# Kernel optimization log

Measured on AMD Instinct MI355X. Metric: run time of the kernel, lower is better.

The kernel has to match this reference:

```python
import jax, jax.numpy as jnp
import numpy as np

B, T, N, V, C, E = 64, 100, 25, 128, 128, 64
EPS = 1e-5


def setup_inputs() -> dict:
    key = jax.random.key(0)
    ks = jax.random.split(key, 6)
    x = jax.random.normal(ks[0], (B, T, N, V), jnp.float32)
    edge_index = jax.random.randint(ks[1], (2, E), 0, N, dtype=jnp.int64)
    W1 = jax.random.normal(ks[2], (V, C), jnp.float32) * (1.0 / np.sqrt(V))
    b1 = jnp.zeros((C,), jnp.float32)
    W2 = jax.random.normal(ks[3], (C, C), jnp.float32) * (1.0 / np.sqrt(C))
    b2 = jnp.zeros((C,), jnp.float32)
    gamma = jnp.ones((T,), jnp.float32)
    beta = jnp.zeros((T,), jnp.float32)
    return {"x": x, "edge_index": edge_index, "W1": W1, "b1": b1,
            "W2": W2, "b2": b2, "gamma": gamma, "beta": beta}


def _gcn_norm(edge_index, n):
    # GCNConv default: add self-loops, symmetric D^{-1/2} A_hat D^{-1/2} norm.
    loop = jnp.arange(n, dtype=edge_index.dtype)
    src = jnp.concatenate([edge_index[0], loop])  # [E + N]
    tgt = jnp.concatenate([edge_index[1], loop])
    deg = jnp.zeros((n,), jnp.float32).at[tgt].add(1.0)
    dis = jax.lax.rsqrt(deg)  # deg >= 1 due to self-loops
    return src, tgt, dis[src] * dis[tgt]


def _gcn_layer(h, W, b, src, tgt, norm):
    # h: [G, N, Cin] -> [G, N, Cout]; linear then gather-scale-scatter aggregate.
    h = jnp.einsum('gnc,cd->gnd', h, W)
    msg = h[:, src, :] * norm[None, :, None]          # [G, E+N, Cout]
    out = jnp.zeros_like(h).at[:, tgt, :].add(msg)    # scatter-add to targets
    return out + b


def reference(x, edge_index, W1, b1, W2, b2, gamma, beta):
    Bv, Tv, Nv, Vv = x.shape
    h = x.reshape(Bv * Tv, Nv, Vv)  # B*T independent graphs, shared edge_index
    src, tgt, norm = _gcn_norm(edge_index, Nv)
    h = _gcn_layer(h, W1, b1, src, tgt, norm)
    h = _gcn_layer(h, W2, b2, src, tgt, norm)
    y = h.reshape(Bv, Tv, Nv, -1)
    # BatchNorm2d(T) in training mode: batch stats over (B, N, C) per T-channel.
    mean = y.mean(axis=(0, 2, 3), keepdims=True)
    var = y.var(axis=(0, 2, 3), keepdims=True)  # biased, matches torch normalization
    y = (y - mean) * jax.lax.rsqrt(var + EPS)
    y = y * gamma[None, :, None, None] + beta[None, :, None, None]
    return jax.nn.relu(y)
```

## Files before the change

### kernel.cpp

```cpp
#include <hip/hip_runtime.h>

#define T_DIM   100
#define N_NODES 25
#define C_DIM   128
#define G_TOTAL 6400
#define GNV     3200
#define TOT_ELEM 20480000
#define CNT_PER_T 204800.0f

#define WS_A2P  0
#define WS_RS1  640
#define WS_BW   768
#define WS_SUM  1024
#define WS_SSQ  1152
#define WS_W12T 2048
#define WS_HB   16384

#define YSTR  36
#define YGSTR (128 * YSTR)

typedef __attribute__((ext_vector_type(8))) short short8;
typedef __attribute__((ext_vector_type(4))) float f32x4;

__device__ __forceinline__ unsigned short f2bf(float f) {
  unsigned int u = __float_as_uint(f);
  u += 0x7FFFu + ((u >> 16) & 1u);
  return (unsigned short)(u >> 16);
}
__device__ __forceinline__ float bf2f(unsigned short h) {
  return __uint_as_float(((unsigned int)h) << 16);
}
__device__ __forceinline__ unsigned int pack2bf(float a, float b) {
  return (unsigned int)f2bf(a) | ((unsigned int)f2bf(b) << 16);
}

__global__ void k_pre(const int* __restrict__ edge, const float* __restrict__ W1,
                      const float* __restrict__ W2, const float* __restrict__ b1,
                      float* __restrict__ wsf) {
  __shared__ float sA[N_NODES * N_NODES];
  __shared__ float sA2[N_NODES * N_NODES];
  __shared__ float sdeg[N_NODES];
  __shared__ float sdis[N_NODES];
  const int tid = threadIdx.x;

  if (blockIdx.x < 64) {
    int j = blockIdx.x * 256 + tid;
    int c = j & 127, v = j >> 7;
    float acc = 0.f;
#pragma unroll 8
    for (int u = 0; u < 128; u++) acc = fmaf(W1[v * 128 + u], W2[u * 128 + c], acc);
    ((unsigned short*)(wsf + WS_W12T))[c * 128 + v] = f2bf(acc);
    if (j < 128) {
      float a2 = 0.f;
      for (int u = 0; u < 128; u++) a2 = fmaf(W2[u * 128 + j], b1[u], a2);
      wsf[WS_BW + j] = a2;
    }
    return;
  }

  if (tid < N_NODES) sdeg[tid] = 0.f;
  for (int j = tid; j < N_NODES * N_NODES; j += 256) sA[j] = 0.f;
  __syncthreads();
  if (tid < 64) atomicAdd(&sdeg[edge[64 + tid]], 1.f);
  __syncthreads();
  if (tid < N_NODES) sdis[tid] = rsqrtf(sdeg[tid] + 1.f);
  __syncthreads();
  if (tid < 64) {
    int s = edge[tid], tg = edge[64 + tid];
    atomicAdd(&sA[tg * N_NODES + s], sdis[s] * sdis[tg]);
  }
  __syncthreads();
  if (tid < N_NODES) atomicAdd(&sA[tid * N_NODES + tid], sdis[tid] * sdis[tid]);
  __syncthreads();
  for (int j = tid; j < N_NODES * N_NODES; j += 256) {
    int n = j / N_NODES, m = j - n * N_NODES;
    float acc = 0.f;
    for (int k = 0; k < N_NODES; k++) acc = fmaf(sA[n * N_NODES + k], sA[k * N_NODES + m], acc);
    sA2[j] = acc;
  }
  __syncthreads();
  for (int j = tid; j < 1024; j += 256) {
    int m = j >> 5, k = j & 31;
    float v = (m < N_NODES && k < N_NODES) ? sA2[m * N_NODES + k] : 0.f;
    ((unsigned short*)(wsf + WS_A2P))[j] = f2bf(v);
  }
  if (tid < N_NODES) {
    float rs = 0.f;
    for (int m = 0; m < N_NODES; m++) rs += sA[tid * N_NODES + m];
    wsf[WS_RS1 + tid] = rs;
  }
  if (tid < T_DIM) { wsf[WS_SUM + tid] = 0.f; wsf[WS_SSQ + tid] = 0.f; }
}

__device__ __forceinline__ void load_a2f(const unsigned short* __restrict__ A2p,
                                         int quad, int l16, short8 a2f[2]) {
#pragma unroll
  for (int mt2 = 0; mt2 < 2; mt2++)
    a2f[mt2] = *(const short8*)&A2p[(mt2 * 16 + l16) * 32 + quad * 8];
}

template <int NT>
__device__ __forceinline__ void stage_x_global(unsigned short* __restrict__ LB,
                                               const float* __restrict__ xb, int tid) {
  for (int j = tid; j < 12 * 128; j += NT) {
    int pr = j >> 7;
    int g = pr / 3, rr = pr - (pr / 3) * 3;
    LB[(g * 28 + 25 + rr) * 128 + (j & 127)] = 0;
  }
  for (int idx = tid; idx < 1600; idx += NT) {
    int row = idx >> 4;
    int c8  = (idx & 15) << 3;
    int g = (row * 41) >> 10;
    int n = row - g * 25;
    const float4* xp = (const float4*)(xb + g * (T_DIM * GNV) + n * 128 + c8);
    float4 f0 = xp[0], f1 = xp[1];
    uint4 w;
    w.x = pack2bf(f0.x, f0.y); w.y = pack2bf(f0.z, f0.w);
    w.z = pack2bf(f1.x, f1.y); w.w = pack2bf(f1.z, f1.w);
    int r = g * 28 + n;
    *(uint4*)&LB[r * 128 + (c8 ^ ((r & 15) << 3))] = w;
  }
}

__device__ __forceinline__ void do_stage2_half(const unsigned short* __restrict__ LB,
    const short8 a2f[2], const float* __restrict__ sBW, const float* __restrict__ sB2,
    const float* __restrict__ rs1, unsigned short* __restrict__ hb, int obase,
    int g, int half, int quad, int l16, float& sum, float& ssq) {
  f32x4 acc2[2][4];
#pragma unroll
  for (int mt2 = 0; mt2 < 2; mt2++)
#pragma unroll
    for (int nt = 0; nt < 4; nt++)
#pragma unroll
      for (int r = 0; r < 4; r++) acc2[mt2][nt][r] = 0.f;

#pragma unroll
  for (int nt = 0; nt < 4; nt++) {
    int c = (half * 4 + nt) * 16 + l16;
    int base = g * YGSTR + c * YSTR + quad * 8;
    uint2 lo = *(const uint2*)&LB[base];
    uint2 hi = *(const uint2*)&LB[base + 4];
    uint4 w; w.x = lo.x; w.y = lo.y; w.z = hi.x; w.w = hi.y;
    short8 bf = __builtin_bit_cast(short8, w);
#pragma unroll
    for (int mt2 = 0; mt2 < 2; mt2++)
      acc2[mt2][nt] = __builtin_amdgcn_mfma_f32_16x16x32_bf16(a2f[mt2], bf, acc2[mt2][nt], 0, 0, 0);
  }
#pragma unroll
  for (int mt2 = 0; mt2 < 2; mt2++) {
#pragma unroll
    for (int nt = 0; nt < 4; nt++) {
      int c = (half * 4 + nt) * 16 + l16;
      float bw = sBW[c], bb = sB2[c];
#pragma unroll
      for (int r = 0; r < 4; r++) {
        int m = mt2 * 16 + quad * 4 + r;
        if (m < N_NODES) {
          float v = acc2[mt2][nt][r] + rs1[m] * bw + bb;
          unsigned short hv = f2bf(v);
          float vq = bf2f(hv);
          hb[obase + m * 128 + c] = hv;
          sum += vq;
          ssq += vq * vq;
        }
      }
    }
  }
}

__global__ __launch_bounds__(512, 8) void k_main_w8(const float* __restrict__ x,
                                                    const float* __restrict__ b2,
                                                    const float* __restrict__ wsc,
                                                    float* __restrict__ stats,
                                                    unsigned short* __restrict__ hb) {
  __shared__ __align__(16) unsigned short LB[4 * YGSTR];
  __shared__ float sBW[128];
  __shared__ float sB2[128];
  __shared__ float rs1[32];
  __shared__ float red[16];
  const int tid = threadIdx.x;
  const int bid = blockIdx.x;
  const int t = bid % T_DIM;
  const int bq = bid / T_DIM;
  const int wv = tid >> 6, lane = tid & 63, quad = lane >> 4, l16 = lane & 15;
  const unsigned short* Wg = (const unsigned short*)(wsc + WS_W12T);
  const unsigned short* A2p = (const unsigned short*)(wsc + WS_A2P);

  if (tid < 128) {
    sBW[tid] = wsc[WS_BW + tid];
    if (tid < N_NODES) rs1[tid] = wsc[WS_RS1 + tid];
  } else if (tid < 256) {
    sB2[tid - 128] = b2[tid - 128];
  }

  stage_x_global<512>(LB, x + (bq * 4 * T_DIM + t) * GNV, tid);

  short8 bfr[4];
  {
    const short8* rp = (const short8*)&Wg[(wv * 16 + l16) * 128];
#pragma unroll
    for (int ks = 0; ks < 4; ks++) bfr[ks] = rp[(ks << 2) | quad];
  }
  __syncthreads();

  f32x4 acc[7];
#pragma unroll
  for (int mt = 0; mt < 7; mt++)
#pragma unroll
    for (int r = 0; r < 4; r++) acc[mt][r] = 0.f;

#pragma unroll
  for (int ks = 0; ks < 4; ks++) {
    const int cc = (ks << 2) | quad;
#pragma unroll
    for (int mt = 0; mt < 7; mt++) {
      int arow = mt * 16 + l16;
      short8 afr = *(const short8*)&LB[arow * 128 + ((cc ^ (arow & 15)) << 3)];
      acc[mt] = __builtin_amdgcn_mfma_f32_16x16x32_bf16(afr, bfr[ks], acc[mt], 0, 0, 0);
    }
  }
  __syncthreads();

#pragma unroll
  for (int mt = 0; mt < 7; mt++) {
    int row0 = mt * 16 + quad * 4;
    int g = row0 / 28;
    int rl = row0 - g * 28;
    int c = wv * 16 + l16;
    uint2 p;
    p.x = pack2bf(acc[mt][0], acc[mt][1]);
    p.y = pack2bf(acc[mt][2], acc[mt][3]);
    *(uint2*)&LB[g * YGSTR + c * YSTR + rl] = p;
  }
  {
    uint2 z; z.x = 0u; z.y = 0u;
    int g = tid >> 7, c = tid & 127;
    *(uint2*)&LB[g * YGSTR + c * YSTR + 28] = z;
  }
  __syncthreads();

  short8 a2f[2];
  load_a2f(A2p, quad, l16, a2f);
  const int g2 = wv >> 1, ch = wv & 1;
  const int obase = ((bq * 4 + g2) * T_DIM + t) * GNV;
  float sum = 0.f, ssq = 0.f;
  do_stage2_half(LB, a2f, sBW, sB2, rs1, hb, obase, g2, ch, quad, l16, sum, ssq);

#pragma unroll
  for (int off = 32; off > 0; off >>= 1) {
    sum += __shfl_down(sum, off, 64);
    ssq += __shfl_down(ssq, off, 64);
  }
  if (lane == 0) { red[wv] = sum; red[8 + wv] = ssq; }
  __syncthreads();
  if (tid == 0) {
    float bs = 0.f, bq2 = 0.f;
#pragma unroll
    for (int w = 0; w < 8; w++) { bs += red[w]; bq2 += red[8 + w]; }
    atomicAdd(&stats[t], bs);
    atomicAdd(&stats[128 + t], bq2);
  }
}

__global__ __launch_bounds__(256) void k_norm_h(const unsigned short* __restrict__ hb,
                                                const float* __restrict__ stats,
                                                const float* __restrict__ gamma,
                                                const float* __restrict__ beta,
                                                float* __restrict__ out) {
  const int i8 = (blockIdx.x * 256 + threadIdx.x) * 8;
  const int t = (i8 / GNV) % T_DIM;
  const float inv = 1.f / CNT_PER_T;
  float s = stats[t], q = stats[128 + t];
  float mean = s * inv;
  float var = fmaf(q, inv, -mean * mean);
  float rstd = rsqrtf(var + 1e-5f);
  float gm = gamma[t] * rstd;
  float bt = fmaf(-mean, gm, beta[t]);
  uint4 hw = *(const uint4*)(hb + i8);
  float4 o0, o1;
  o0.x = fmaxf(fmaf(bf2f((unsigned short)(hw.x & 0xFFFF)), gm, bt), 0.f);
  o0.y = fmaxf(fmaf(bf2f((unsigned short)(hw.x >> 16)),    gm, bt), 0.f);
  o0.z = fmaxf(fmaf(bf2f((unsigned short)(hw.y & 0xFFFF)), gm, bt), 0.f);
  o0.w = fmaxf(fmaf(bf2f((unsigned short)(hw.y >> 16)),    gm, bt), 0.f);
  o1.x = fmaxf(fmaf(bf2f((unsigned short)(hw.z & 0xFFFF)), gm, bt), 0.f);
  o1.y = fmaxf(fmaf(bf2f((unsigned short)(hw.z >> 16)),    gm, bt), 0.f);
  o1.z = fmaxf(fmaf(bf2f((unsigned short)(hw.w & 0xFFFF)), gm, bt), 0.f);
  o1.w = fmaxf(fmaf(bf2f((unsigned short)(hw.w >> 16)),    gm, bt), 0.f);
  *(float4*)(out + i8) = o0;
  *(float4*)(out + i8 + 4) = o1;
}

__global__ __launch_bounds__(256, 4) void k_main_f(const float* __restrict__ x,
                                                   const float* __restrict__ b2,
                                                   const float* __restrict__ wsc,
                                                   float* __restrict__ stats,
                                                   float* __restrict__ outf) {
  __shared__ __align__(16) unsigned short LB[4 * YGSTR];
  __shared__ float sBW[128];
  __shared__ float sB2[128];
  __shared__ float rs1[32];
  __shared__ float red[8];
  const int tid = threadIdx.x;
  const int bid = blockIdx.x;
  const int t = bid % T_DIM;
  const int bq = bid / T_DIM;
  const int wv = tid >> 6, lane = tid & 63, quad = lane >> 4, l16 = lane & 15;
  const unsigned short* Wg = (const unsigned short*)(wsc + WS_W12T);
  const unsigned short* A2p = (const unsigned short*)(wsc + WS_A2P);

  if (tid < 128) {
    sBW[tid] = wsc[WS_BW + tid];
    if (tid < N_NODES) rs1[tid] = wsc[WS_RS1 + tid];
  } else {
    sB2[tid - 128] = b2[tid - 128];
  }
  stage_x_global<256>(LB, x + (bq * 4 * T_DIM + t) * GNV, tid);
  short8 bfr[2][4];
  {
#pragma unroll
    for (int nt = 0; nt < 2; nt++) {
      const short8* rp = (const short8*)&Wg[(wv * 32 + nt * 16 + l16) * 128];
#pragma unroll
      for (int ks = 0; ks < 4; ks++) bfr[nt][ks] = rp[(ks << 2) | quad];
    }
  }
  __syncthreads();
  f32x4 acc[7][2];
#pragma unroll
  for (int mt = 0; mt < 7; mt++)
#pragma unroll
    for (int nt = 0; nt < 2; nt++)
#pragma unroll
      for (int r = 0; r < 4; r++) acc[mt][nt][r] = 0.f;
#pragma unroll
  for (int ks = 0; ks < 4; ks++) {
    const int cc = (ks << 2) | quad;
#pragma unroll
    for (int mt = 0; mt < 7; mt++) {
      int arow = mt * 16 + l16;
      short8 afr = *(const short8*)&LB[arow * 128 + ((cc ^ (arow & 15)) << 3)];
#pragma unroll
      for (int nt = 0; nt < 2; nt++)
        acc[mt][nt] = __builtin_amdgcn_mfma_f32_16x16x32_bf16(afr, bfr[nt][ks], acc[mt][nt], 0, 0, 0);
    }
  }
  __syncthreads();
#pragma unroll
  for (int mt = 0; mt < 7; mt++) {
    int row0 = mt * 16 + quad * 4;
    int g = row0 / 28;
    int rl = row0 - g * 28;
#pragma unroll
    for (int nt = 0; nt < 2; nt++) {
      int c = wv * 32 + nt * 16 + l16;
      uint2 p;
      p.x = pack2bf(acc[mt][nt][0], acc[mt][nt][1]);
      p.y = pack2bf(acc[mt][nt][2], acc[mt][nt][3]);
      *(uint2*)&LB[g * YGSTR + c * YSTR + rl] = p;
    }
  }
  {
    uint2 z; z.x = 0u; z.y = 0u;
    for (int j = tid; j < 512; j += 256) {
      int g = j >> 7, c = j & 127;
      *(uint2*)&LB[g * YGSTR + c * YSTR + 28] = z;
    }
  }
  __syncthreads();
  short8 a2f[2];
  load_a2f(A2p, quad, l16, a2f);
  const int obase = ((bq * 4 + wv) * T_DIM + t) * GNV;
  float sum = 0.f, ssq = 0.f;
#pragma unroll
  for (int half = 0; half < 2; half++) {
    f32x4 acc2[2][4];
#pragma unroll
    for (int mt2 = 0; mt2 < 2; mt2++)
#pragma unroll
      for (int nt = 0; nt < 4; nt++)
#pragma unroll
        for (int r = 0; r < 4; r++) acc2[mt2][nt][r] = 0.f;
#pragma unroll
    for (int nt = 0; nt < 4; nt++) {
      int c = (half * 4 + nt) * 16 + l16;
      int base = wv * YGSTR + c * YSTR + quad * 8;
      uint2 lo = *(const uint2*)&LB[base];
      uint2 hi = *(const uint2*)&LB[base + 4];
      uint4 w; w.x = lo.x; w.y = lo.y; w.z = hi.x; w.w = hi.y;
      short8 bf = __builtin_bit_cast(short8, w);
#pragma unroll
      for (int mt2 = 0; mt2 < 2; mt2++)
        acc2[mt2][nt] = __builtin_amdgcn_mfma_f32_16x16x32_bf16(a2f[mt2], bf, acc2[mt2][nt], 0, 0, 0);
    }
#pragma unroll
    for (int mt2 = 0; mt2 < 2; mt2++) {
#pragma unroll
      for (int nt = 0; nt < 4; nt++) {
        int c = (half * 4 + nt) * 16 + l16;
        float bw = sBW[c], bb = sB2[c];
#pragma unroll
        for (int r = 0; r < 4; r++) {
          int m = mt2 * 16 + quad * 4 + r;
          if (m < N_NODES) {
            float v = acc2[mt2][nt][r] + rs1[m] * bw + bb;
            outf[obase + m * 128 + c] = v;
            sum += v;
            ssq += v * v;
          }
        }
      }
    }
  }
#pragma unroll
  for (int off = 32; off > 0; off >>= 1) {
    sum += __shfl_down(sum, off, 64);
    ssq += __shfl_down(ssq, off, 64);
  }
  if (lane == 0) { red[wv] = sum; red[4 + wv] = ssq; }
  __syncthreads();
  if (tid == 0) {
    atomicAdd(&stats[t], red[0] + red[1] + red[2] + red[3]);
    atomicAdd(&stats[128 + t], red[4] + red[5] + red[6] + red[7]);
  }
}

#define NORM_STR  1280000
__global__ __launch_bounds__(256) void k_norm_f(float* __restrict__ out,
                                                const float* __restrict__ stats,
                                                const float* __restrict__ gamma,
                                                const float* __restrict__ beta) {
  const int i0 = blockIdx.x * 256 + threadIdx.x;
  const float inv = 1.f / CNT_PER_T;
  float4 h[4];
  float g[4], bb[4];
  int base[4];
#pragma unroll
  for (int k = 0; k < 4; k++) {
    int i4 = i0 + k * NORM_STR;
    base[k] = i4 * 4;
    int t = (base[k] / GNV) % T_DIM;
    float s = stats[t], q = stats[128 + t];
    float mean = s * inv;
    float var = fmaf(q, inv, -mean * mean);
    float rstd = rsqrtf(var + 1e-5f);
    g[k] = gamma[t] * rstd;
    bb[k] = fmaf(-mean, g[k], beta[t]);
    h[k] = *(const float4*)(out + base[k]);
  }
#pragma unroll
  for (int k = 0; k < 4; k++) {
    float4 v = h[k];
    v.x = fmaxf(fmaf(v.x, g[k], bb[k]), 0.f);
    v.y = fmaxf(fmaf(v.y, g[k], bb[k]), 0.f);
    v.z = fmaxf(fmaf(v.z, g[k], bb[k]), 0.f);
    v.w = fmaxf(fmaf(v.w, g[k], bb[k]), 0.f);
    *(float4*)(out + base[k]) = v;
  }
}

extern "C" void kernel_launch(void* const* d_in, const int* in_sizes, int n_in,
                              void* d_out, int out_size, void* d_ws, size_t ws_size,
                              hipStream_t stream) {
  const float* x     = (const float*)d_in[0];
  const int*   edge  = (const int*)d_in[1];
  const float* W1    = (const float*)d_in[2];
  const float* b1    = (const float*)d_in[3];
  const float* W2    = (const float*)d_in[4];
  const float* b2    = (const float*)d_in[5];
  const float* gamma = (const float*)d_in[6];
  const float* beta  = (const float*)d_in[7];
  float* out = (float*)d_out;
  float* wsf = (float*)d_ws;

  k_pre<<<65, 256, 0, stream>>>(edge, W1, W2, b1, wsf);

  const size_t need = (size_t)WS_HB * 4 + (size_t)TOT_ELEM * 2;
  if (ws_size >= need) {
    unsigned short* hb = (unsigned short*)(wsf + WS_HB);
    k_main_w8<<<G_TOTAL / 4, 512, 0, stream>>>(x, b2, wsf, wsf + WS_SUM, hb);
    k_norm_h<<<TOT_ELEM / (256 * 8), 256, 0, stream>>>(hb, wsf + WS_SUM, gamma, beta, out);
  } else {
    k_main_f<<<G_TOTAL / 4, 256, 0, stream>>>(x, b2, wsf, wsf + WS_SUM, out);
    k_norm_f<<<NORM_STR / 256, 256, 0, stream>>>(out, wsf + WS_SUM, gamma, beta);
  }
}
```

Measured before the change: 199.8 us.

## Process two graphs per block with 256 threads instead of four with 512

The main fused GCN kernel now handles 2 graphs per block with 4 waves instead of 4 graphs with 8 waves, so the grid doubles and LDS per block halves. Each wave now computes two 16-column groups over 4 row tiles instead of one group over 7 tiles, and the zero-padding and x staging are rewritten for the 2-graph layout. The aim is finer-grained scheduling and more resident blocks per CU. The cost is twice as many stats atomics, and the B-fragment (weight) loads per graph double.

After: 201.6 us. About the same (+0.9%).

```diff
diff --git a/kernel.cpp b/kernel.cpp
--- a/kernel.cpp
+++ b/kernel.cpp
@@ -99,29 +99,6 @@
     a2f[mt2] = *(const short8*)&A2p[(mt2 * 16 + l16) * 32 + quad * 8];
 }
 
-template <int NT>
-__device__ __forceinline__ void stage_x_global(unsigned short* __restrict__ LB,
-                                               const float* __restrict__ xb, int tid) {
-  for (int j = tid; j < 12 * 128; j += NT) {
-    int pr = j >> 7;
-    int g = pr / 3, rr = pr - (pr / 3) * 3;
-    LB[(g * 28 + 25 + rr) * 128 + (j & 127)] = 0;
-  }
-  for (int idx = tid; idx < 1600; idx += NT) {
-    int row = idx >> 4;
-    int c8  = (idx & 15) << 3;
-    int g = (row * 41) >> 10;
-    int n = row - g * 25;
-    const float4* xp = (const float4*)(xb + g * (T_DIM * GNV) + n * 128 + c8);
-    float4 f0 = xp[0], f1 = xp[1];
-    uint4 w;
-    w.x = pack2bf(f0.x, f0.y); w.y = pack2bf(f0.z, f0.w);
-    w.z = pack2bf(f1.x, f1.y); w.w = pack2bf(f1.z, f1.w);
-    int r = g * 28 + n;
-    *(uint4*)&LB[r * 128 + (c8 ^ ((r & 15) << 3))] = w;
-  }
-}
-
 __device__ __forceinline__ void do_stage2_half(const unsigned short* __restrict__ LB,
     const short8 a2f[2], const float* __restrict__ sBW, const float* __restrict__ sB2,
     const float* __restrict__ rs1, unsigned short* __restrict__ hb, int obase,
@@ -168,20 +145,20 @@
   }
 }
 
-__global__ __launch_bounds__(512, 8) void k_main_w8(const float* __restrict__ x,
+__global__ __launch_bounds__(256, 8) void k_main_g2(const float* __restrict__ x,
                                                     const float* __restrict__ b2,
                                                     const float* __restrict__ wsc,
                                                     float* __restrict__ stats,
                                                     unsigned short* __restrict__ hb) {
-  __shared__ __align__(16) unsigned short LB[4 * YGSTR];
+  __shared__ __align__(16) unsigned short LB[2 * YGSTR];
   __shared__ float sBW[128];
   __shared__ float sB2[128];
   __shared__ float rs1[32];
-  __shared__ float red[16];
+  __shared__ float red[8];
   const int tid = threadIdx.x;
   const int bid = blockIdx.x;
   const int t = bid % T_DIM;
-  const int bq = bid / T_DIM;
+  const int bp = bid / T_DIM;
   const int wv = tid >> 6, lane = tid & 63, quad = lane >> 4, l16 = lane & 15;
   const unsigned short* Wg = (const unsigned short*)(wsc + WS_W12T);
   const unsigned short* A2p = (const unsigned short*)(wsc + WS_A2P);
@@ -189,48 +166,76 @@
   if (tid < 128) {
     sBW[tid] = wsc[WS_BW + tid];
     if (tid < N_NODES) rs1[tid] = wsc[WS_RS1 + tid];
-  } else if (tid < 256) {
+  } else {
     sB2[tid - 128] = b2[tid - 128];
   }
 
-  stage_x_global<512>(LB, x + (bq * 4 * T_DIM + t) * GNV, tid);
-
-  short8 bfr[4];
+  for (int j = tid; j < 14 * 128; j += 256) {
+    int pr = j >> 7;
+    int row = (pr < 3) ? 25 + pr : 50 + pr;
+    LB[row * 128 + (j & 127)] = 0;
+  }
+
   {
-    const short8* rp = (const short8*)&Wg[(wv * 16 + l16) * 128];
+    const float* xb = x + (bp * 2 * T_DIM + t) * GNV;
+    for (int idx = tid; idx < 800; idx += 256) {
+      int row = idx >> 4;
+      int c8  = (idx & 15) << 3;
+      int g = (row >= 25) ? 1 : 0;
+      int n = row - g * 25;
+      const float4* xp = (const float4*)(xb + g * (T_DIM * GNV) + n * 128 + c8);
+      float4 f0 = xp[0], f1 = xp[1];
+      uint4 w;
+      w.x = pack2bf(f0.x, f0.y); w.y = pack2bf(f0.z, f0.w);
+      w.z = pack2bf(f1.x, f1.y); w.w = pack2bf(f1.z, f1.w);
+      int r = g * 28 + n;
+      *(uint4*)&LB[r * 128 + (c8 ^ ((r & 15) << 3))] = w;
+    }
+  }
+  __syncthreads();
+
+  f32x4 acc[2][4];
+#pragma unroll
+  for (int cg = 0; cg < 2; cg++)
+#pragma unroll
+    for (int mt = 0; mt < 4; mt++)
+#pragma unroll
+      for (int r = 0; r < 4; r++) acc[cg][mt][r] = 0.f;
+
+#pragma unroll
+  for (int cg = 0; cg < 2; cg++) {
+    short8 bfr[4];
+    const short8* rp = (const short8*)&Wg[(wv * 32 + cg * 16 + l16) * 128];
 #pragma unroll
     for (int ks = 0; ks < 4; ks++) bfr[ks] = rp[(ks << 2) | quad];
-  }
-  __syncthreads();
-
-  f32x4 acc[7];
-#pragma unroll
-  for (int mt = 0; mt < 7; mt++)
-#pragma unroll
-    for (int r = 0; r < 4; r++) acc[mt][r] = 0.f;
-
-#pragma unroll
-  for (int ks = 0; ks < 4; ks++) {
-    const int cc = (ks << 2) | quad;
-#pragma unroll
-    for (int mt = 0; mt < 7; mt++) {
-      int arow = mt * 16 + l16;
-      short8 afr = *(const short8*)&LB[arow * 128 + ((cc ^ (arow & 15)) << 3)];
-      acc[mt] = __builtin_amdgcn_mfma_f32_16x16x32_bf16(afr, bfr[ks], acc[mt], 0, 0, 0);
-    }
-  }
-  __syncthreads();
-
-#pragma unroll
-  for (int mt = 0; mt < 7; mt++) {
-    int row0 = mt * 16 + quad * 4;
-    int g = row0 / 28;
-    int rl = row0 - g * 28;
-    int c = wv * 16 + l16;
-    uint2 p;
-    p.x = pack2bf(acc[mt][0], acc[mt][1]);
-    p.y = pack2bf(acc[mt][2], acc[mt][3]);
-    *(uint2*)&LB[g * YGSTR + c * YSTR + rl] = p;
+#pragma unroll
+    for (int ks = 0; ks < 4; ks++) {
+      const int cc = (ks << 2) | quad;
+#pragma unroll
+      for (int mt = 0; mt < 4; mt++) {
+        int arow = mt * 16 + l16;
+        short8 afr = *(const short8*)&LB[arow * 128 + ((cc ^ (arow & 15)) << 3)];
+        acc[cg][mt] = __builtin_amdgcn_mfma_f32_16x16x32_bf16(afr, bfr[ks], acc[cg][mt], 0, 0, 0);
+      }
+    }
+  }
+  __syncthreads();
+
+#pragma unroll
+  for (int cg = 0; cg < 2; cg++) {
+#pragma unroll
+    for (int mt = 0; mt < 4; mt++) {
+      int row0 = mt * 16 + quad * 4;
+      if (row0 < 56) {
+        int g = (row0 >= 28) ? 1 : 0;
+        int rl = row0 - g * 28;
+        int c = wv * 32 + cg * 16 + l16;
+        uint2 p;
+        p.x = pack2bf(acc[cg][mt][0], acc[cg][mt][1]);
+        p.y = pack2bf(acc[cg][mt][2], acc[cg][mt][3]);
+        *(uint2*)&LB[g * YGSTR + c * YSTR + rl] = p;
+      }
+    }
   }
   {
     uint2 z; z.x = 0u; z.y = 0u;
@@ -242,7 +247,7 @@
   short8 a2f[2];
   load_a2f(A2p, quad, l16, a2f);
   const int g2 = wv >> 1, ch = wv & 1;
-  const int obase = ((bq * 4 + g2) * T_DIM + t) * GNV;
+  const int obase = ((bp * 2 + g2) * T_DIM + t) * GNV;
   float sum = 0.f, ssq = 0.f;
   do_stage2_half(LB, a2f, sBW, sB2, rs1, hb, obase, g2, ch, quad, l16, sum, ssq);
 
@@ -251,14 +256,11 @@
     sum += __shfl_down(sum, off, 64);
     ssq += __shfl_down(ssq, off, 64);
   }
-  if (lane == 0) { red[wv] = sum; red[8 + wv] = ssq; }
+  if (lane == 0) { red[wv] = sum; red[4 + wv] = ssq; }
   __syncthreads();
   if (tid == 0) {
-    float bs = 0.f, bq2 = 0.f;
-#pragma unroll
-    for (int w = 0; w < 8; w++) { bs += red[w]; bq2 += red[8 + w]; }
-    atomicAdd(&stats[t], bs);
-    atomicAdd(&stats[128 + t], bq2);
+    atomicAdd(&stats[t], red[0] + red[1] + red[2] + red[3]);
+    atomicAdd(&stats[128 + t], red[4] + red[5] + red[6] + red[7]);
   }
 }
 
@@ -290,6 +292,29 @@
   *(float4*)(out + i8 + 4) = o1;
 }
 
+template <int NT>
+__device__ __forceinline__ void stage_x_global4(unsigned short* __restrict__ LB,
+                                                const float* __restrict__ xb, int tid) {
+  for (int j = tid; j < 12 * 128; j += NT) {
+    int pr = j >> 7;
+    int g = pr / 3, rr = pr - (pr / 3) * 3;
+    LB[(g * 28 + 25 + rr) * 128 + (j & 127)] = 0;
+  }
+  for (int idx = tid; idx < 1600; idx += NT) {
+    int row = idx >> 4;
+    int c8  = (idx & 15) << 3;
+    int g = (row * 41) >> 10;
+    int n = row - g * 25;
+    const float4* xp = (const float4*)(xb + g * (T_DIM * GNV) + n * 128 + c8);
+    float4 f0 = xp[0], f1 = xp[1];
+    uint4 w;
+    w.x = pack2bf(f0.x, f0.y); w.y = pack2bf(f0.z, f0.w);
+    w.z = pack2bf(f1.x, f1.y); w.w = pack2bf(f1.z, f1.w);
+    int r = g * 28 + n;
+    *(uint4*)&LB[r * 128 + (c8 ^ ((r & 15) << 3))] = w;
+  }
+}
+
 __global__ __launch_bounds__(256, 4) void k_main_f(const float* __restrict__ x,
                                                    const float* __restrict__ b2,
                                                    const float* __restrict__ wsc,
@@ -314,7 +339,7 @@
   } else {
     sB2[tid - 128] = b2[tid - 128];
   }
-  stage_x_global<256>(LB, x + (bq * 4 * T_DIM + t) * GNV, tid);
+  stage_x_global4<256>(LB, x + (bq * 4 * T_DIM + t) * GNV, tid);
   short8 bfr[2][4];
   {
 #pragma unroll
@@ -477,7 +502,7 @@
   const size_t need = (size_t)WS_HB * 4 + (size_t)TOT_ELEM * 2;
   if (ws_size >= need) {
     unsigned short* hb = (unsigned short*)(wsf + WS_HB);
-    k_main_w8<<<G_TOTAL / 4, 512, 0, stream>>>(x, b2, wsf, wsf + WS_SUM, hb);
+    k_main_g2<<<G_TOTAL / 2, 256, 0, stream>>>(x, b2, wsf, wsf + WS_SUM, hb);
     k_norm_h<<<TOT_ELEM / (256 * 8), 256, 0, stream>>>(hb, wsf + WS_SUM, gamma, beta, out);
   } else {
     k_main_f<<<G_TOTAL / 4, 256, 0, stream>>>(x, b2, wsf, wsf + WS_SUM, out);
```
